# Kernel optimization log

Measured on AMD Instinct MI355X. Metric: run time of the kernel, lower is better.

## Reference

```python
import jax, jax.numpy as jnp
import numpy as np

VOL_SHAPE = (160, 192, 160)

def setup_inputs() -> dict:
    key = jax.random.key(0)
    k1, k2 = jax.random.split(key)
    vol = jax.random.normal(k1, (2, *VOL_SHAPE, 1), dtype=jnp.float32)
    trf = jax.random.normal(k2, (2, *VOL_SHAPE, 3), dtype=jnp.float32)
    return {"vol": vol, "trf": trf}

def _warp(vol, trf):
    # vol: [B, X, Y, Z, C]; trf: [B, X, Y, Z, 3] dense displacement field ('ij' indexing)
    B = vol.shape[0]
    shape = vol.shape[1:-1]
    nd = len(shape)
    # sample locations = identity grid + displacement
    grid = jnp.stack(jnp.meshgrid(*[jnp.arange(s, dtype=vol.dtype) for s in shape], indexing='ij'), axis=-1)
    loc = grid[None] + trf  # [B, X, Y, Z, 3]
    max_f = jnp.array([s - 1 for s in shape], dtype=vol.dtype)
    max_i = jnp.array([s - 1 for s in shape], dtype=jnp.int32)
    # fill_value=None -> clamp to volume border (voxelmorph interpn semantics)
    loc = jnp.clip(loc, 0.0, max_f)
    loc0f = jnp.floor(loc)
    loc0 = jnp.clip(loc0f.astype(jnp.int32), 0, max_i)        # lower corner indices
    loc1 = jnp.clip(loc0 + 1, 0, max_i)                       # upper corner indices (clipped)
    d1 = loc1.astype(vol.dtype) - loc                          # weight for lower corner
    d0 = 1.0 - d1                                              # weight for upper corner
    b = jnp.arange(B)[:, None, None, None]
    out = jnp.zeros(vol.shape, dtype=vol.dtype)
    for c in range(2 ** nd):                                   # 8 corners, fixed small loop
        bits = [(c >> d) & 1 for d in range(nd)]
        idx = [loc1[..., d] if bits[d] else loc0[..., d] for d in range(nd)]
        w = jnp.ones(loc.shape[:-1], dtype=vol.dtype)
        for d in range(nd):
            w = w * (d0[..., d] if bits[d] else d1[..., d])
        out = out + w[..., None] * vol[b, idx[0], idx[1], idx[2]]
    return out

def reference(vol, trf):
    return _warp(vol, trf)
```

## Files before the change

kernel.cpp:

```cpp
#include <hip/hip_runtime.h>


#define NXD 160
#define NYD 192
#define NZD 160
#define NVOX (NXD * NYD * NZD)
#define NBATCH 2

#define TXT 8
#define TYT 16
#define TZT 16
#define LXT 16
#define LYT 24
#define LZT 32
#define LDS_N (LXT * LYT * LZT)

#define TILES_X (NXD / TXT)
#define TILES_Y (NYD / TYT)
#define TILES_Z (NZD / TZT)
#define NBLOCKS (NBATCH * TILES_X * TILES_Y * TILES_Z)

typedef float f4 __attribute__((ext_vector_type(4)));

__global__ __launch_bounds__(512)
void warp3d_kernel(const float* __restrict__ vol,
                   const float* __restrict__ trf,
                   float* __restrict__ out) {
    __shared__ float tile[LDS_N];

    int bid = blockIdx.x;
    int tz = bid % TILES_Z;
    int r  = bid / TILES_Z;
    int ty = r % TILES_Y;
    int r2 = r / TILES_Y;
    int tx = r2 % TILES_X;
    int b  = r2 / TILES_X;

    int x0t = tx * TXT, y0t = ty * TYT, z0t = tz * TZT;
    int lox = min(max(x0t - 4, 0), NXD - LXT);
    int loy = min(max(y0t - 4, 0), NYD - LYT);
    int loz = min(max(z0t - 8, 0), NZD - LZT);

    const float* vb = vol + (size_t)b * NVOX;

    int t = threadIdx.x;
    int zq = t & 3;
    int yq = (t >> 2) & 15;
    int xq = t >> 6;
    int x = x0t + xq, y = y0t + yq, zb0 = z0t + zq * 4;
    size_t vox_i = (((size_t)b * NXD + x) * NYD + y) * NZD + zb0;

    const f4* trfv = (const f4*)(trf + vox_i * 3);
    f4 t0 = trfv[0], t1 = trfv[1], t2 = trfv[2];

    {
        const float* gbase = vb + ((size_t)(lox * NYD + loy) * NZD + loz);
        int w = t >> 6;
        int l = t & 63;
        int zgrp = (l & 7) << 2;
        int lrow = l >> 3;
#pragma unroll
        for (int it = 0; it < 6; ++it) {
            int chunk = it * 8 + w;
            int rest = chunk * 8 + lrow;
            int yi = rest % LYT;
            int xi = rest / LYT;
            int sz = zgrp ^ ((yi & 7) << 2);
            const float* g = gbase + (size_t)xi * (NYD * NZD) + yi * NZD + sz;
            __builtin_amdgcn_global_load_lds(
                (const __attribute__((address_space(1))) void*)g,
                (__attribute__((address_space(3))) void*)&tile[chunk * 256],
                16, 0, 0);
        }
    }
    __syncthreads();

    float dxa[4] = {t0.x, t0.w, t1.z, t2.y};
    float dya[4] = {t0.y, t1.x, t1.w, t2.z};
    float dza[4] = {t0.z, t1.y, t2.x, t2.w};

    float res[4];
#pragma unroll
    for (int j = 0; j < 4; ++j) {
        float lx = fminf(fmaxf((float)x + dxa[j], 0.0f), (float)(NXD - 1));
        float ly = fminf(fmaxf((float)y + dya[j], 0.0f), (float)(NYD - 1));
        float lz = fminf(fmaxf((float)(zb0 + j) + dza[j], 0.0f), (float)(NZD - 1));
        float fx = floorf(lx), fy = floorf(ly), fz = floorf(lz);
        int x0 = (int)fx, y0 = (int)fy, z0 = (int)fz;
        float wx0 = fminf(fx + 1.0f, (float)(NXD - 1)) - lx;
        float wy0 = fminf(fy + 1.0f, (float)(NYD - 1)) - ly;
        float wz0 = fminf(fz + 1.0f, (float)(NZD - 1)) - lz;

        int ix = x0 - lox, iy = y0 - loy, iz = z0 - loz;
        bool ok = ((unsigned)ix <= LXT - 2) & ((unsigned)iy <= LYT - 2) &
                  ((unsigned)iz <= LZT - 2);
        int sx = ok ? ix : 0;
        int sy = ok ? iy : 0;
        int sv = ok ? iz : 0;

        int r00 = (sx * LYT + sy) * LZT;
        int r01 = r00 + LZT;
        int r10 = r00 + LYT * LZT;
        int r11 = r10 + LZT;
        int sw0 = (sy & 7) << 2;
        int sw1 = ((sy + 1) & 7) << 2;
        int za = sv ^ sw0, zb = (sv + 1) ^ sw0;
        int zc = sv ^ sw1, zd = (sv + 1) ^ sw1;

        float v000 = tile[r00 + za], v001 = tile[r00 + zb];
        float v010 = tile[r01 + zc], v011 = tile[r01 + zd];
        float v100 = tile[r10 + za], v101 = tile[r10 + zb];
        float v110 = tile[r11 + zc], v111 = tile[r11 + zd];

        if (!ok) {
            int x1 = min(x0 + 1, NXD - 1);
            int y1 = min(y0 + 1, NYD - 1);
            int z1 = min(z0 + 1, NZD - 1);
            size_t o00 = (size_t)(x0 * NYD + y0) * NZD;
            size_t o01 = (size_t)(x0 * NYD + y1) * NZD;
            size_t o10 = (size_t)(x1 * NYD + y0) * NZD;
            size_t o11 = (size_t)(x1 * NYD + y1) * NZD;
            v000 = vb[o00 + z0]; v001 = vb[o00 + z1];
            v010 = vb[o01 + z0]; v011 = vb[o01 + z1];
            v100 = vb[o10 + z0]; v101 = vb[o10 + z1];
            v110 = vb[o11 + z0]; v111 = vb[o11 + z1];
        }

        float wx1 = 1.0f - wx0, wy1 = 1.0f - wy0, wz1 = 1.0f - wz0;
        res[j] = wx0 * (wy0 * (wz0 * v000 + wz1 * v001) +
                        wy1 * (wz0 * v010 + wz1 * v011)) +
                 wx1 * (wy0 * (wz0 * v100 + wz1 * v101) +
                        wy1 * (wz0 * v110 + wz1 * v111));
    }

    f4 o;
    o.x = res[0]; o.y = res[1]; o.z = res[2]; o.w = res[3];
    *(f4*)(out + vox_i) = o;
}

extern "C" void kernel_launch(void* const* d_in, const int* in_sizes, int n_in,
                              void* d_out, int out_size, void* d_ws, size_t ws_size,
                              hipStream_t stream) {
    const float* vol = (const float*)d_in[0];
    const float* trf = (const float*)d_in[1];
    float* out = (float*)d_out;

    warp3d_kernel<<<NBLOCKS, 512, 0, stream>>>(vol, trf, out);
}
```

Baseline: 223.0 us.

## Interleave z voxels across threads and overlap index math with LDS tile load

Each thread now handles four voxels strided by 4 in z instead of four contiguous ones, so trf loads and output stores become scalar strided accesses that are coalesced across lanes rather than 16-byte vector loads. Coordinate, weight and LDS index computation move before the __syncthreads so they overlap the asynchronous global-to-LDS tile fill. Fallback paths recompute corner indices from trf rather than keeping them in registers. This trades vector memory ops for more instructions, and holding the precomputed indices and weights may raise register pressure.

```diff
diff --git a/kernel.cpp b/kernel.cpp
--- a/kernel.cpp
+++ b/kernel.cpp
@@ -19,8 +19,6 @@
 #define TILES_Y (NYD / TYT)
 #define TILES_Z (NZD / TZT)
 #define NBLOCKS (NBATCH * TILES_X * TILES_Y * TILES_Z)
-
-typedef float f4 __attribute__((ext_vector_type(4)));
 
 __global__ __launch_bounds__(512)
 void warp3d_kernel(const float* __restrict__ vol,
@@ -47,11 +45,18 @@
     int zq = t & 3;
     int yq = (t >> 2) & 15;
     int xq = t >> 6;
-    int x = x0t + xq, y = y0t + yq, zb0 = z0t + zq * 4;
-    size_t vox_i = (((size_t)b * NXD + x) * NYD + y) * NZD + zb0;
+    int x = x0t + xq, y = y0t + yq;
+    int zb0 = z0t + zq;
+    size_t rowi = (((size_t)b * NXD + x) * NYD + y) * NZD + zb0;
+    const float* tp = trf + rowi * 3;
 
-    const f4* trfv = (const f4*)(trf + vox_i * 3);
-    f4 t0 = trfv[0], t1 = trfv[1], t2 = trfv[2];
+    float dxa[4], dya[4], dza[4];
+#pragma unroll
+    for (int j = 0; j < 4; ++j) {
+        dxa[j] = tp[j * 12 + 0];
+        dya[j] = tp[j * 12 + 1];
+        dza[j] = tp[j * 12 + 2];
+    }
 
     {
         const float* gbase = vb + ((size_t)(lox * NYD + loy) * NZD + loz);
@@ -73,46 +78,52 @@
                 16, 0, 0);
         }
     }
-    __syncthreads();
 
-    float dxa[4] = {t0.x, t0.w, t1.z, t2.y};
-    float dya[4] = {t0.y, t1.x, t1.w, t2.z};
-    float dza[4] = {t0.z, t1.y, t2.x, t2.w};
-
-    float res[4];
+    int A[4], B[4], C[4], D[4];
+    float WX[4], WY[4], WZ[4];
+    int okbits = 0;
 #pragma unroll
     for (int j = 0; j < 4; ++j) {
         float lx = fminf(fmaxf((float)x + dxa[j], 0.0f), (float)(NXD - 1));
         float ly = fminf(fmaxf((float)y + dya[j], 0.0f), (float)(NYD - 1));
-        float lz = fminf(fmaxf((float)(zb0 + j) + dza[j], 0.0f), (float)(NZD - 1));
+        float lz = fminf(fmaxf((float)(zb0 + 4 * j) + dza[j], 0.0f), (float)(NZD - 1));
         float fx = floorf(lx), fy = floorf(ly), fz = floorf(lz);
         int x0 = (int)fx, y0 = (int)fy, z0 = (int)fz;
-        float wx0 = fminf(fx + 1.0f, (float)(NXD - 1)) - lx;
-        float wy0 = fminf(fy + 1.0f, (float)(NYD - 1)) - ly;
-        float wz0 = fminf(fz + 1.0f, (float)(NZD - 1)) - lz;
-
+        WX[j] = fminf(fx + 1.0f, (float)(NXD - 1)) - lx;
+        WY[j] = fminf(fy + 1.0f, (float)(NYD - 1)) - ly;
+        WZ[j] = fminf(fz + 1.0f, (float)(NZD - 1)) - lz;
         int ix = x0 - lox, iy = y0 - loy, iz = z0 - loz;
         bool ok = ((unsigned)ix <= LXT - 2) & ((unsigned)iy <= LYT - 2) &
                   ((unsigned)iz <= LZT - 2);
+        okbits |= ((int)ok) << j;
         int sx = ok ? ix : 0;
         int sy = ok ? iy : 0;
         int sv = ok ? iz : 0;
-
-        int r00 = (sx * LYT + sy) * LZT;
-        int r01 = r00 + LZT;
-        int r10 = r00 + LYT * LZT;
-        int r11 = r10 + LZT;
+        int base = (sx * LYT + sy) * LZT;
         int sw0 = (sy & 7) << 2;
         int sw1 = ((sy + 1) & 7) << 2;
-        int za = sv ^ sw0, zb = (sv + 1) ^ sw0;
-        int zc = sv ^ sw1, zd = (sv + 1) ^ sw1;
+        A[j] = base + (sv ^ sw0);
+        B[j] = base + ((sv + 1) ^ sw0);
+        C[j] = base + (sv ^ sw1);
+        D[j] = base + ((sv + 1) ^ sw1);
+    }
+    __syncthreads();
 
-        float v000 = tile[r00 + za], v001 = tile[r00 + zb];
-        float v010 = tile[r01 + zc], v011 = tile[r01 + zd];
-        float v100 = tile[r10 + za], v101 = tile[r10 + zb];
-        float v110 = tile[r11 + zc], v111 = tile[r11 + zd];
+#pragma unroll
+    for (int j = 0; j < 4; ++j) {
+        float v000 = tile[A[j]],                  v001 = tile[B[j]];
+        float v010 = tile[C[j] + LZT],            v011 = tile[D[j] + LZT];
+        float v100 = tile[A[j] + LYT * LZT],      v101 = tile[B[j] + LYT * LZT];
+        float v110 = tile[C[j] + LYT * LZT + LZT], v111 = tile[D[j] + LYT * LZT + LZT];
 
-        if (!ok) {
+        if (!((okbits >> j) & 1)) {
+            float dx = tp[j * 12 + 0];
+            float dy = tp[j * 12 + 1];
+            float dz = tp[j * 12 + 2];
+            float lx = fminf(fmaxf((float)x + dx, 0.0f), (float)(NXD - 1));
+            float ly = fminf(fmaxf((float)y + dy, 0.0f), (float)(NYD - 1));
+            float lz = fminf(fmaxf((float)(zb0 + 4 * j) + dz, 0.0f), (float)(NZD - 1));
+            int x0 = (int)floorf(lx), y0 = (int)floorf(ly), z0 = (int)floorf(lz);
             int x1 = min(x0 + 1, NXD - 1);
             int y1 = min(y0 + 1, NYD - 1);
             int z1 = min(z0 + 1, NZD - 1);
@@ -126,16 +137,14 @@
             v110 = vb[o11 + z0]; v111 = vb[o11 + z1];
         }
 
+        float wx0 = WX[j], wy0 = WY[j], wz0 = WZ[j];
         float wx1 = 1.0f - wx0, wy1 = 1.0f - wy0, wz1 = 1.0f - wz0;
-        res[j] = wx0 * (wy0 * (wz0 * v000 + wz1 * v001) +
-                        wy1 * (wz0 * v010 + wz1 * v011)) +
-                 wx1 * (wy0 * (wz0 * v100 + wz1 * v101) +
-                        wy1 * (wz0 * v110 + wz1 * v111));
+        float res = wx0 * (wy0 * (wz0 * v000 + wz1 * v001) +
+                           wy1 * (wz0 * v010 + wz1 * v011)) +
+                    wx1 * (wy0 * (wz0 * v100 + wz1 * v101) +
+                           wy1 * (wz0 * v110 + wz1 * v111));
+        out[rowi + 4 * j] = res;
     }
-
-    f4 o;
-    o.x = res[0]; o.y = res[1]; o.z = res[2]; o.w = res[3];
-    *(f4*)(out + vox_i) = o;
 }
 
 extern "C" void kernel_launch(void* const* d_in, const int* in_sizes, int n_in,
```

New measurement: 239.4 us. 7.3% more time.

## Shrink LDS halo tile and reswizzle to fit more blocks per CU

Applied to the files above, without the earlier changes.

Reduces the staged LDS tile from 16x24x32 to 14x22x32 by trimming the x/y halo from 4 to 3 voxels. This cuts LDS per block so more 512-thread blocks can be resident, and the launch bounds now request that residency. The staging loop switches from 16-byte to 4-byte direct global-to-LDS loads with a full-width z^y XOR swizzle, and the eight-corner lookup is rewritten to match. The trade-offs are more load instructions for the fill, narrower memory transactions, and more voxels falling back to scattered global gathers because the halo is smaller.

```diff
diff --git a/kernel.cpp b/kernel.cpp
--- a/kernel.cpp
+++ b/kernel.cpp
@@ -10,10 +10,11 @@
 #define TXT 8
 #define TYT 16
 #define TZT 16
-#define LXT 16
-#define LYT 24
+#define LXT 14
+#define LYT 22
 #define LZT 32
-#define LDS_N (LXT * LYT * LZT)
+#define NROWS (LXT * LYT)
+#define LDS_N (NROWS * LZT)
 
 #define TILES_X (NXD / TXT)
 #define TILES_Y (NYD / TYT)
@@ -22,7 +23,7 @@
 
 typedef float f4 __attribute__((ext_vector_type(4)));
 
-__global__ __launch_bounds__(512)
+__global__ __launch_bounds__(512, 8)
 void warp3d_kernel(const float* __restrict__ vol,
                    const float* __restrict__ trf,
                    float* __restrict__ out) {
@@ -37,8 +38,8 @@
     int b  = r2 / TILES_X;
 
     int x0t = tx * TXT, y0t = ty * TYT, z0t = tz * TZT;
-    int lox = min(max(x0t - 4, 0), NXD - LXT);
-    int loy = min(max(y0t - 4, 0), NYD - LYT);
+    int lox = min(max(x0t - 3, 0), NXD - LXT);
+    int loy = min(max(y0t - 3, 0), NYD - LYT);
     int loz = min(max(z0t - 8, 0), NZD - LZT);
 
     const float* vb = vol + (size_t)b * NVOX;
@@ -54,23 +55,25 @@
     f4 t0 = trfv[0], t1 = trfv[1], t2 = trfv[2];
 
     {
+        int zi = t & 31;
+        int yi = t >> 5;
+        int rowoff = yi * NZD;
         const float* gbase = vb + ((size_t)(lox * NYD + loy) * NZD + loz);
-        int w = t >> 6;
-        int l = t & 63;
-        int zgrp = (l & 7) << 2;
-        int lrow = l >> 3;
 #pragma unroll
-        for (int it = 0; it < 6; ++it) {
-            int chunk = it * 8 + w;
-            int rest = chunk * 8 + lrow;
-            int yi = rest % LYT;
-            int xi = rest / LYT;
-            int sz = zgrp ^ ((yi & 7) << 2);
-            const float* g = gbase + (size_t)xi * (NYD * NZD) + yi * NZD + sz;
-            __builtin_amdgcn_global_load_lds(
-                (const __attribute__((address_space(1))) void*)g,
-                (__attribute__((address_space(3))) void*)&tile[chunk * 256],
-                16, 0, 0);
+        for (int it = 0; it < 20; ++it) {
+            int row = it * 16 + (t >> 5);
+            if (row < NROWS) {
+                const float* g = gbase + rowoff + (zi ^ yi);
+                __builtin_amdgcn_global_load_lds(
+                    (const __attribute__((address_space(1))) void*)g,
+                    (__attribute__((address_space(3))) void*)
+                        &tile[(it * 16 + ((t >> 6) << 1)) * LZT],
+                    4, 0, 0);
+            }
+            yi += 16;
+            int wrap = yi >= LYT;
+            rowoff += wrap ? (16 * NZD - LYT * NZD + NYD * NZD) : 16 * NZD;
+            if (wrap) yi -= LYT;
         }
     }
     __syncthreads();
@@ -98,19 +101,16 @@
         int sy = ok ? iy : 0;
         int sv = ok ? iz : 0;
 
-        int r00 = (sx * LYT + sy) * LZT;
-        int r01 = r00 + LZT;
-        int r10 = r00 + LYT * LZT;
-        int r11 = r10 + LZT;
-        int sw0 = (sy & 7) << 2;
-        int sw1 = ((sy + 1) & 7) << 2;
-        int za = sv ^ sw0, zb = (sv + 1) ^ sw0;
-        int zc = sv ^ sw1, zd = (sv + 1) ^ sw1;
+        int base = (sx * LYT + sy) * LZT;
+        int A = base + (sv ^ sy);
+        int B = base + ((sv + 1) ^ sy);
+        int C = base + LZT + (sv ^ (sy + 1));
+        int D = base + LZT + ((sv + 1) ^ (sy + 1));
 
-        float v000 = tile[r00 + za], v001 = tile[r00 + zb];
-        float v010 = tile[r01 + zc], v011 = tile[r01 + zd];
-        float v100 = tile[r10 + za], v101 = tile[r10 + zb];
-        float v110 = tile[r11 + zc], v111 = tile[r11 + zd];
+        float v000 = tile[A],              v001 = tile[B];
+        float v010 = tile[C],              v011 = tile[D];
+        float v100 = tile[A + LYT * LZT],  v101 = tile[B + LYT * LZT];
+        float v110 = tile[C + LYT * LZT],  v111 = tile[D + LYT * LZT];
 
         if (!ok) {
             int x1 = min(x0 + 1, NXD - 1);
```

After: 243.7 us. 1.09x slower.
